# Performance work log

Measured on AMD Instinct MI355X. Metric: run time of the kernel, lower is better.

Reference implementation:

```python
import jax, jax.numpy as jnp
import numpy as np

B, N, DIN, D, NH, NL = 4, 256, 4, 64, 4, 2
DH = D // NH
EPS = 1e-5
SLOPE = 0.01  # torch LeakyReLU default negative_slope


def setup_inputs() -> dict:
    key = jax.random.key(0)
    ks = jax.random.split(key, 16)
    def p(k, shape, s=0.05):
        return jax.random.normal(k, shape, jnp.float32) * s
    return {
        "feature": jax.random.normal(ks[0], (B, N, N, DIN), jnp.float32),
        "W1": p(ks[1], (DIN, D)), "b1": jnp.zeros((D,), jnp.float32),
        "mw": p(ks[2], (NH, D)), "mb": jnp.zeros((NH,), jnp.float32),
        "bn_gamma": jnp.ones((D,), jnp.float32), "bn_beta": jnp.zeros((D,), jnp.float32),
        "Wq": p(ks[3], (NL, D, D)), "bq": jnp.zeros((NL, D), jnp.float32),
        "Wk": p(ks[4], (NL, D, D)), "bk": jnp.zeros((NL, D), jnp.float32),
        "Wv": p(ks[5], (NL, D, D)), "bv": jnp.zeros((NL, D), jnp.float32),
        "Wo": p(ks[6], (NL, D, D)), "bo": jnp.zeros((NL, D), jnp.float32),
        "ln1_g": jnp.ones((NL, D), jnp.float32), "ln1_b": jnp.zeros((NL, D), jnp.float32),
        "Wff1": p(ks[7], (NL, D, 2 * D)), "bff1": jnp.zeros((NL, 2 * D), jnp.float32),
        "Wff2": p(ks[8], (NL, 2 * D, D)), "bff2": jnp.zeros((NL, D), jnp.float32),
        "ln2_g": jnp.ones((NL, D), jnp.float32), "ln2_b": jnp.zeros((NL, D), jnp.float32),
    }


def _leaky(x):
    return jnp.where(x >= 0, x, SLOPE * x)


def _layer_norm(x, g, b):
    m = x.mean(axis=-1, keepdims=True)
    v = x.var(axis=-1, keepdims=True)
    return g * (x - m) / jnp.sqrt(v + EPS) + b


def reference(feature, W1, b1, mw, mb, bn_gamma, bn_beta,
              Wq, bq, Wk, bk, Wv, bv, Wo, bo, ln1_g, ln1_b,
              Wff1, bff1, Wff2, bff2, ln2_g, ln2_b):
    # linear1: (B,N,N,DIN) -> (B,N,N,D)
    feat = feature @ W1 + b1
    # per-head scalar attention score over node pairs: (NH,B,N,N)
    s = jnp.einsum('bijh,nh->nbij', feat, mw) + mb[:, None, None, None]
    w = jnp.exp(_leaky(s))
    w = w / w.sum(axis=3, keepdims=True)  # softmax-like over second node dim j
    # weighted aggregation: sum over i, then mean over heads -> (B,N,D)
    h = jnp.einsum('nbij,bijh->bjh', w, feat) / NH
    # BatchNorm1d over channels D, stats over (B,N) (training-mode, biased var)
    m = h.mean(axis=(0, 1))
    v = h.var(axis=(0, 1))
    x = bn_gamma * (h - m) / jnp.sqrt(v + EPS) + bn_beta  # (B,N,D)
    # standard post-LN TransformerEncoder, NL layers
    scale = 1.0 / np.sqrt(DH).astype(np.float32)
    for l in range(NL):
        q = (x @ Wq[l] + bq[l]).reshape(B, N, NH, DH)
        k = (x @ Wk[l] + bk[l]).reshape(B, N, NH, DH)
        vv = (x @ Wv[l] + bv[l]).reshape(B, N, NH, DH)
        a = jax.nn.softmax(jnp.einsum('bqhd,bkhd->bhqk', q, k) * scale, axis=-1)
        o = jnp.einsum('bhqk,bkhd->bqhd', a, vv).reshape(B, N, D) @ Wo[l] + bo[l]
        x = _layer_norm(x + o, ln1_g[l], ln1_b[l])
        f = jax.nn.relu(x @ Wff1[l] + bff1[l]) @ Wff2[l] + bff2[l]
        x = _layer_norm(x + f, ln2_g[l], ln2_b[l])
    return x
```

## Files before the change

### kernel.cpp

```cpp
#include <hip/hip_runtime.h>
#include <math.h>

#define B 4
#define N 256
#define DIN 4
#define D 64
#define NH 4
#define NL 2
#define DH 16

constexpr float EPS = 1e-5f;
constexpr float SLOPE = 0.01f;

template <int NF4>
__device__ __forceinline__ void stage(float* dst, const float* src, int t) {
    int lane = t & 63, w = t >> 6;
#pragma unroll
    for (int i0 = 0; i0 < NF4; i0 += 512) {
        int base = i0 + w * 64;
        __builtin_amdgcn_global_load_lds(
            (const __attribute__((address_space(1))) void*)(src + 4 * (base + lane)),
            (__attribute__((address_space(3))) void*)(dst + 4 * base),
            16, 0, 0);
    }
}

__global__ void __launch_bounds__(256) k_rowsum(
    const float* __restrict__ feature, const float* __restrict__ W1,
    const float* __restrict__ b1, const float* __restrict__ mw,
    const float* __restrict__ mb, float* __restrict__ rs,
    float* __restrict__ bnacc ) {
    __shared__ float M[16];
    __shared__ float C[4];
    int t = threadIdx.x;
    int lane = t & 63, w = t >> 6;
    int cb = blockIdx.x;
    if (cb == 0 && t < 128) bnacc[t] = 0.f;
    if (t < 16) {
        int n = t >> 2, kk = t & 3;
        float s = 0.f;
        for (int d = 0; d < D; ++d) s += W1[kk * D + d] * mw[n * D + d];
        M[t] = s;
    } else if (t < 20) {
        int n = t - 16;
        float s = mb[n];
        for (int d = 0; d < D; ++d) s += b1[d] * mw[n * D + d];
        C[n] = s;
    }
    __syncthreads();

    int bi = cb * 4 + w;
    const float4* fb = (const float4*)(feature) + (size_t)bi * N;
    float sn[4] = {0.f, 0.f, 0.f, 0.f};
#pragma unroll
    for (int m = 0; m < 4; ++m) {
        float4 f = fb[lane + 64 * m];
#pragma unroll
        for (int n = 0; n < 4; ++n) {
            float s = C[n] + f.x * M[n*4+0] + f.y * M[n*4+1] + f.z * M[n*4+2] + f.w * M[n*4+3];
            s = (s >= 0.f) ? s : SLOPE * s;
            sn[n] += __expf(s);
        }
    }
#pragma unroll
    for (int n = 0; n < 4; ++n)
#pragma unroll
        for (int off = 32; off > 0; off >>= 1) sn[n] += __shfl_xor(sn[n], off);
    if (lane == 0) {
        float4 o = {sn[0], sn[1], sn[2], sn[3]};
        *(float4*)(rs + (size_t)bi * 4) = o;
    }
}

__global__ void __launch_bounds__(256) k_aggregate(
    const float* __restrict__ feature, const float* __restrict__ W1,
    const float* __restrict__ b1, const float* __restrict__ mw,
    const float* __restrict__ mb, const float* __restrict__ rs,
    float* __restrict__ h, float* __restrict__ bnacc) {
    __shared__ float M[16];
    __shared__ float C[4];
    __shared__ float part[80];
    __shared__ float gacc[20];
    __shared__ float hs[4][D];
    int t = threadIdx.x;
    int lane = t & 63, w = t >> 6;
    int cb = blockIdx.x;
    if (t < 16) {
        int n = t >> 2, kk = t & 3;
        float s = 0.f;
        for (int d = 0; d < D; ++d) s += W1[kk * D + d] * mw[n * D + d];
        M[t] = s;
    } else if (t < 20) {
        int n = t - 16;
        float s = mb[n];
        for (int d = 0; d < D; ++d) s += b1[d] * mw[n * D + d];
        C[n] = s;
    }
    __syncthreads();

    int b = cb >> 6, j0 = (cb & 63) * 4;
    int i = t;
    const float4* fb = (const float4*)(feature) + ((size_t)(b * N + i) * N + j0);
    float4 f[4];
#pragma unroll
    for (int jj = 0; jj < 4; ++jj) f[jj] = fb[jj];
    float4 r4 = *(const float4*)(rs + (size_t)(b * N + i) * 4);
    float rinv[4] = {1.f / r4.x, 1.f / r4.y, 1.f / r4.z, 1.f / r4.w};
    float acc[4][5];
#pragma unroll
    for (int jj = 0; jj < 4; ++jj) {
        float wbar = 0.f;
#pragma unroll
        for (int n = 0; n < 4; ++n) {
            float s = C[n] + f[jj].x * M[n*4+0] + f[jj].y * M[n*4+1] + f[jj].z * M[n*4+2] + f[jj].w * M[n*4+3];
            s = (s >= 0.f) ? s : SLOPE * s;
            wbar += __expf(s) * rinv[n];
        }
        wbar *= 0.25f;
        acc[jj][0] = wbar * f[jj].x; acc[jj][1] = wbar * f[jj].y;
        acc[jj][2] = wbar * f[jj].z; acc[jj][3] = wbar * f[jj].w;
        acc[jj][4] = wbar;
    }
#pragma unroll
    for (int jj = 0; jj < 4; ++jj)
#pragma unroll
        for (int c = 0; c < 5; ++c)
#pragma unroll
            for (int off = 32; off > 0; off >>= 1) acc[jj][c] += __shfl_xor(acc[jj][c], off);
    if (lane == 0) {
#pragma unroll
        for (int jj = 0; jj < 4; ++jj)
#pragma unroll
            for (int c = 0; c < 5; ++c) part[w * 20 + jj * 5 + c] = acc[jj][c];
    }
    __syncthreads();
    if (t < 20) gacc[t] = part[t] + part[20 + t] + part[40 + t] + part[60 + t];
    __syncthreads();
    float hv = gacc[w * 5 + 4] * b1[lane];
#pragma unroll
    for (int kk = 0; kk < 4; ++kk) hv += gacc[w * 5 + kk] * W1[kk * D + lane];
    h[((size_t)(b * N + j0 + w)) * D + lane] = hv;
    hs[w][lane] = hv;
    __syncthreads();
    if (w == 0) {
        float s = hs[0][lane] + hs[1][lane] + hs[2][lane] + hs[3][lane];
        float sq = hs[0][lane]*hs[0][lane] + hs[1][lane]*hs[1][lane]
                 + hs[2][lane]*hs[2][lane] + hs[3][lane]*hs[3][lane];
        atomicAdd(bnacc + lane, s);
        atomicAdd(bnacc + D + lane, sq);
    }
}

__global__ void __launch_bounds__(512, 2) k_qkv0(
    const float* __restrict__ h, const float* __restrict__ bnacc,
    const float* __restrict__ bn_g, const float* __restrict__ bn_b,
    const float* __restrict__ Wq, const float* __restrict__ bq,
    const float* __restrict__ Wk, const float* __restrict__ bk,
    const float* __restrict__ Wv, const float* __restrict__ bv,
    float* __restrict__ x, float* __restrict__ q,
    float* __restrict__ k, float* __restrict__ v) {
    __shared__ __align__(16) float xsh[4 * D];
    __shared__ __align__(16) float pp[8 * 192];
    __shared__ __align__(16) float WqL[D * D];
    __shared__ __align__(16) float WkL[D * D];
    __shared__ __align__(16) float WvL[D * D];
    int t = threadIdx.x;
    int lane = t & 63, w = t >> 6;
    int tok4 = w & 3, kh = w >> 2;
    int token = blockIdx.x * 4 + tok4;
    int b = token >> 8, n = token & (N - 1);
    int ch = lane;

    stage<D * D / 4>(WqL, Wq, t);
    stage<D * D / 4>(WkL, Wk, t);
    stage<D * D / 4>(WvL, Wv, t);

    float mean = bnacc[ch] * (1.0f / (B * N));
    float var = bnacc[D + ch] * (1.0f / (B * N)) - mean * mean;
    float inv = rsqrtf(var + EPS);
    size_t xi = (size_t)token * D + ch;
    float xv = bn_g[ch] * (h[xi] - mean) * inv + bn_b[ch];
    float bq_r = bq[ch], bk_r = bk[ch], bv_r = bv[ch];
    if (kh == 0) {
        x[xi] = xv;
        xsh[tok4 * D + ch] = xv;
    }
    __syncthreads();

    const float4* xr4 = (const float4*)(xsh + tok4 * D + kh * 32);
    float aq0=0.f, aq1=0.f, ak0=0.f, ak1=0.f, av0=0.f, av1=0.f;
#pragma unroll
    for (int k4 = 0; k4 < 8; ++k4) {
        float4 xx = xr4[k4];
        int kk = kh * 32 + k4 * 4;
        aq0 += xx.x * WqL[(kk+0)*D+ch] + xx.z * WqL[(kk+2)*D+ch];
        aq1 += xx.y * WqL[(kk+1)*D+ch] + xx.w * WqL[(kk+3)*D+ch];
        ak0 += xx.x * WkL[(kk+0)*D+ch] + xx.z * WkL[(kk+2)*D+ch];
        ak1 += xx.y * WkL[(kk+1)*D+ch] + xx.w * WkL[(kk+3)*D+ch];
        av0 += xx.x * WvL[(kk+0)*D+ch] + xx.z * WvL[(kk+2)*D+ch];
        av1 += xx.y * WvL[(kk+1)*D+ch] + xx.w * WvL[(kk+3)*D+ch];
    }
    float* ppw = pp + w * 192;
    ppw[ch] = aq0 + aq1;
    ppw[64 + ch] = ak0 + ak1;
    ppw[128 + ch] = av0 + av1;
    __syncthreads();
    if (kh == 0) {
        int head = ch >> 4, dh = ch & (DH - 1);
        size_t oidx = (((size_t)(b * NH + head)) * N + n) * DH + dh;
        q[oidx] = bq_r + pp[tok4*192 + ch] + pp[(tok4+4)*192 + ch];
        k[oidx] = bk_r + pp[tok4*192 + 64 + ch] + pp[(tok4+4)*192 + 64 + ch];
        v[oidx] = bv_r + pp[tok4*192 + 128 + ch] + pp[(tok4+4)*192 + 128 + ch];
    }
}

__global__ void __launch_bounds__(512, 2) k_layer(
    const float* __restrict__ q, const float* __restrict__ k,
    const float* __restrict__ v,
    const float* __restrict__ Wo, const float* __restrict__ bo,
    const float* __restrict__ ln1g, const float* __restrict__ ln1b,
    const float* __restrict__ Wff1, const float* __restrict__ bff1,
    const float* __restrict__ Wff2, const float* __restrict__ bff2,
    const float* __restrict__ ln2g, const float* __restrict__ ln2b,
    const float* __restrict__ Wqn, const float* __restrict__ bqn,
    const float* __restrict__ Wkn, const float* __restrict__ bkn,
    const float* __restrict__ Wvn, const float* __restrict__ bvn,
    float* __restrict__ qo, float* __restrict__ ko, float* __restrict__ vo,
    float* __restrict__ x) {
    __shared__ __align__(16) float attS[4 * D];
    __shared__ __align__(16) float xs1[4 * D];
    __shared__ __align__(16) float f1s[4 * 2 * D];
    __shared__ __align__(16) float pp[8 * 192];
    __shared__ __align__(16) float WoL[D * D];
    __shared__ __align__(16) float Wff1L[D * 2 * D];
    __shared__ __align__(16) float Wff2L[2 * D * D];
    __shared__ __align__(16) float WqnL[D * D];
    __shared__ __align__(16) float WknL[D * D];
    __shared__ __align__(16) float WvnL[D * D];

    int t = threadIdx.x;
    int lane = t & 63, w = t >> 6;
    int b = blockIdx.x;
    int q0 = blockIdx.y * 4;
    int h_ = w & 3, qpair = w >> 2;
    int tok4 = w & 3, kh = w >> 2;
    int token = q0 + tok4;
    int ch = lane;

    int bh = b * NH + h_;
    const float* kb = k + (size_t)bh * N * DH;
    const float* vb = v + (size_t)bh * N * DH;
    float4 Kr[4][4], Vr[4][4];
#pragma unroll
    for (int j = 0; j < 4; ++j) {
        int key = lane + 64 * j;
#pragma unroll
        for (int c = 0; c < 4; ++c) {
            Kr[j][c] = *(const float4*)(kb + (size_t)key * DH + 4 * c);
            Vr[j][c] = *(const float4*)(vb + (size_t)key * DH + 4 * c);
        }
    }

    size_t xidx = ((size_t)b * N + token) * D + ch;
    float xv = x[xidx];
    float bo_r = bo[ch], l1g = ln1g[ch], l1b = ln1b[ch];
    float bf1_r = bff1[kh * D + ch];
    float bf2_r = bff2[ch], l2g = ln2g[ch], l2b = ln2b[ch];
    float bq_r = 0.f, bk_r = 0.f, bv_r = 0.f;
    if (Wqn != nullptr) { bq_r = bqn[ch]; bk_r = bkn[ch]; bv_r = bvn[ch]; }

    stage<1024>(WoL, Wo, t);
    stage<2048>(Wff1L, Wff1, t);
    stage<2048>(Wff2L, Wff2, t);
    if (Wqn != nullptr) {
        stage<1024>(WqnL, Wqn, t);
        stage<1024>(WknL, Wkn, t);
        stage<1024>(WvnL, Wvn, t);
    }

#pragma unroll
    for (int qq2 = 0; qq2 < 2; ++qq2) {
        int qq = qpair * 2 + qq2;
        const float* qp = q + ((size_t)bh * N + q0 + qq) * DH;
        float sq[DH];
#pragma unroll
        for (int d = 0; d < DH; ++d) sq[d] = qp[d];
        float s[4];
#pragma unroll
        for (int j = 0; j < 4; ++j) {
            float a = 0.f;
#pragma unroll
            for (int c = 0; c < 4; ++c)
                a += sq[4*c+0]*Kr[j][c].x + sq[4*c+1]*Kr[j][c].y +
                     sq[4*c+2]*Kr[j][c].z + sq[4*c+3]*Kr[j][c].w;
            s[j] = a;
        }
        float m = fmaxf(fmaxf(s[0], s[1]), fmaxf(s[2], s[3]));
#pragma unroll
        for (int off = 32; off > 0; off >>= 1) m = fmaxf(m, __shfl_xor(m, off));
        float p[4], lsum = 0.f;
#pragma unroll
        for (int j = 0; j < 4; ++j) { p[j] = __expf((s[j] - m) * 0.25f); lsum += p[j]; }
#pragma unroll
        for (int off = 32; off > 0; off >>= 1) lsum += __shfl_xor(lsum, off);
        float o[DH];
#pragma unroll
        for (int d = 0; d < DH; ++d) o[d] = 0.f;
#pragma unroll
        for (int j = 0; j < 4; ++j) {
#pragma unroll
            for (int c = 0; c < 4; ++c) {
                o[4*c+0] += p[j] * Vr[j][c].x;
                o[4*c+1] += p[j] * Vr[j][c].y;
                o[4*c+2] += p[j] * Vr[j][c].z;
                o[4*c+3] += p[j] * Vr[j][c].w;
            }
        }
#pragma unroll
        for (int d = 0; d < DH; ++d) {
#pragma unroll
            for (int off = 32; off > 0; off >>= 1) o[d] += __shfl_xor(o[d], off);
        }
        if (lane == 0) {
            float rl = 1.f / lsum;
#pragma unroll
            for (int d = 0; d < DH; ++d) attS[qq * D + h_ * DH + d] = o[d] * rl;
        }
    }
    __syncthreads();

    float* ppw = pp + w * 192;
    {
        const float4* ar4 = (const float4*)(attS + tok4 * D + kh * 32);
        float a0=0.f, a1=0.f, a2=0.f, a3=0.f;
#pragma unroll
        for (int k4 = 0; k4 < 8; ++k4) {
            float4 av = ar4[k4];
            int kk = kh * 32 + k4 * 4;
            a0 += av.x * WoL[(kk+0)*D+ch];
            a1 += av.y * WoL[(kk+1)*D+ch];
            a2 += av.z * WoL[(kk+2)*D+ch];
            a3 += av.w * WoL[(kk+3)*D+ch];
        }
        ppw[ch] = (a0+a1)+(a2+a3);
    }
    __syncthreads();
    float oo = bo_r + pp[tok4*192 + ch] + pp[(tok4+4)*192 + ch];
    float r = xv + oo;
    float s1 = r, sq1 = r * r;
#pragma unroll
    for (int off = 32; off > 0; off >>= 1) {
        s1 += __shfl_xor(s1, off);
        sq1 += __shfl_xor(sq1, off);
    }
    float mean1 = s1 * (1.0f / D);
    float var1 = sq1 * (1.0f / D) - mean1 * mean1;
    float x1 = l1g * (r - mean1) * rsqrtf(var1 + EPS) + l1b;
    if (kh == 0) xs1[tok4 * D + ch] = x1;
    __syncthreads();

    {
        const float4* xr4 = (const float4*)(xs1 + tok4 * D + kh * 32);
        float u0=0.f,u1=0.f,u2=0.f,u3=0.f, g0=0.f,g1=0.f,g2=0.f,g3=0.f;
#pragma unroll
        for (int k4 = 0; k4 < 8; ++k4) {
            float4 xx = xr4[k4];
            int kk = kh * 32 + k4 * 4;
            u0 += xx.x * Wff1L[(kk+0)*128+ch];
            u1 += xx.y * Wff1L[(kk+1)*128+ch];
            u2 += xx.z * Wff1L[(kk+2)*128+ch];
            u3 += xx.w * Wff1L[(kk+3)*128+ch];
            g0 += xx.x * Wff1L[(kk+0)*128+64+ch];
            g1 += xx.y * Wff1L[(kk+1)*128+64+ch];
            g2 += xx.z * Wff1L[(kk+2)*128+64+ch];
            g3 += xx.w * Wff1L[(kk+3)*128+64+ch];
        }
        ppw[ch] = (u0+u1)+(u2+u3);
        ppw[64+ch] = (g0+g1)+(g2+g3);
    }
    __syncthreads();
    f1s[tok4*128 + kh*64 + ch] =
        fmaxf(pp[tok4*192 + kh*64 + ch] + pp[(tok4+4)*192 + kh*64 + ch] + bf1_r, 0.f);
    __syncthreads();

    {
        const float4* fr4 = (const float4*)(f1s + tok4*128 + kh*64);
        float e0=0.f,e1=0.f,e2=0.f,e3=0.f;
#pragma unroll
        for (int k4 = 0; k4 < 16; ++k4) {
            float4 fv = fr4[k4];
            int kk = kh*64 + k4*4;
            e0 += fv.x * Wff2L[(kk+0)*D+ch];
            e1 += fv.y * Wff2L[(kk+1)*D+ch];
            e2 += fv.z * Wff2L[(kk+2)*D+ch];
            e3 += fv.w * Wff2L[(kk+3)*D+ch];
        }
        ppw[ch] = (e0+e1)+(e2+e3);
    }
    __syncthreads();
    float o2 = bf2_r + pp[tok4*192 + ch] + pp[(tok4+4)*192 + ch];
    float r2 = x1 + o2;
    float s2 = r2, sq2 = r2 * r2;
#pragma unroll
    for (int off = 32; off > 0; off >>= 1) {
        s2 += __shfl_xor(s2, off);
        sq2 += __shfl_xor(sq2, off);
    }
    float mean2 = s2 * (1.0f / D);
    float var2 = sq2 * (1.0f / D) - mean2 * mean2;
    float xnew = l2g * (r2 - mean2) * rsqrtf(var2 + EPS) + l2b;
    if (kh == 0) x[xidx] = xnew;

    if (Wqn != nullptr) {
        if (kh == 0) attS[tok4 * D + ch] = xnew;
        __syncthreads();
        const float4* xr4 = (const float4*)(attS + tok4 * D + kh * 32);
        float aq0=0.f, aq1=0.f, ak0=0.f, ak1=0.f, av0=0.f, av1=0.f;
#pragma unroll
        for (int k4 = 0; k4 < 8; ++k4) {
            float4 xx = xr4[k4];
            int kk = kh * 32 + k4 * 4;
            aq0 += xx.x * WqnL[(kk+0)*D+ch] + xx.z * WqnL[(kk+2)*D+ch];
            aq1 += xx.y * WqnL[(kk+1)*D+ch] + xx.w * WqnL[(kk+3)*D+ch];
            ak0 += xx.x * WknL[(kk+0)*D+ch] + xx.z * WknL[(kk+2)*D+ch];
            ak1 += xx.y * WknL[(kk+1)*D+ch] + xx.w * WknL[(kk+3)*D+ch];
            av0 += xx.x * WvnL[(kk+0)*D+ch] + xx.z * WvnL[(kk+2)*D+ch];
            av1 += xx.y * WvnL[(kk+1)*D+ch] + xx.w * WvnL[(kk+3)*D+ch];
        }
        ppw[ch] = aq0 + aq1;
        ppw[64+ch] = ak0 + ak1;
        ppw[128+ch] = av0 + av1;
        __syncthreads();
        if (kh == 0) {
            int head = ch >> 4, dh = ch & (DH - 1);
            size_t oidx = (((size_t)(b * NH + head)) * N + token) * DH + dh;
            qo[oidx] = bq_r + pp[tok4*192 + ch] + pp[(tok4+4)*192 + ch];
            ko[oidx] = bk_r + pp[tok4*192 + 64 + ch] + pp[(tok4+4)*192 + 64 + ch];
            vo[oidx] = bv_r + pp[tok4*192 + 128 + ch] + pp[(tok4+4)*192 + 128 + ch];
        }
    }
}

extern "C" void kernel_launch(void* const* d_in, const int* in_sizes, int n_in,
                              void* d_out, int out_size, void* d_ws, size_t ws_size,
                              hipStream_t stream) {
    const float* feature = (const float*)d_in[0];
    const float* W1   = (const float*)d_in[1];
    const float* b1   = (const float*)d_in[2];
    const float* mw   = (const float*)d_in[3];
    const float* mb   = (const float*)d_in[4];
    const float* bn_g = (const float*)d_in[5];
    const float* bn_b = (const float*)d_in[6];
    const float* Wq   = (const float*)d_in[7];
    const float* bq   = (const float*)d_in[8];
    const float* Wk   = (const float*)d_in[9];
    const float* bk   = (const float*)d_in[10];
    const float* Wv   = (const float*)d_in[11];
    const float* bv   = (const float*)d_in[12];
    const float* Wo   = (const float*)d_in[13];
    const float* bo   = (const float*)d_in[14];
    const float* ln1g = (const float*)d_in[15];
    const float* ln1b = (const float*)d_in[16];
    const float* Wff1 = (const float*)d_in[17];
    const float* bff1 = (const float*)d_in[18];
    const float* Wff2 = (const float*)d_in[19];
    const float* bff2 = (const float*)d_in[20];
    const float* ln2g = (const float*)d_in[21];
    const float* ln2b = (const float*)d_in[22];

    float* ws    = (float*)d_ws;
    float* rs    = ws;
    float* h     = rs + B * N * NH;
    float* bnacc = h + B * N * D;
    float* q     = bnacc + 128;
    float* k     = q + B * N * D;
    float* v     = k + B * N * D;
    float* x     = (float*)d_out;

    k_rowsum<<<256, 256, 0, stream>>>(feature, W1, b1, mw, mb, rs, bnacc);
    k_aggregate<<<256, 256, 0, stream>>>(feature, W1, b1, mw, mb, rs, h, bnacc);
    k_qkv0<<<256, 512, 0, stream>>>(h, bnacc, bn_g, bn_b,
                                    Wq, bq, Wk, bk, Wv, bv, x, q, k, v);
    k_layer<<<dim3(B, N / 4), 512, 0, stream>>>(q, k, v,
        Wo, bo, ln1g, ln1b, Wff1, bff1, Wff2, bff2, ln2g, ln2b,
        Wq + (size_t)D * D, bq + D, Wk + (size_t)D * D, bk + D,
        Wv + (size_t)D * D, bv + D, q, k, v, x);
    k_layer<<<dim3(B, N / 4), 512, 0, stream>>>(q, k, v,
        Wo + (size_t)D * D, bo + D, ln1g + D, ln1b + D,
        Wff1 + (size_t)D * 2 * D, bff1 + 2 * D,
        Wff2 + (size_t)2 * D * D, bff2 + D, ln2g + D, ln2b + D,
        nullptr, nullptr, nullptr, nullptr, nullptr, nullptr,
        nullptr, nullptr, nullptr, x);
}
```

Measured before the change: 147.8 us.

## Double threads in rowsum/aggregate and split attention keys across waves

Result: slower. 156.5 us (+5.9%).

```diff
diff --git a/kernel.cpp b/kernel.cpp
--- a/kernel.cpp
+++ b/kernel.cpp
@@ -25,13 +25,14 @@
     }
 }
 
-__global__ void __launch_bounds__(256) k_rowsum(
+__global__ void __launch_bounds__(512) k_rowsum(
     const float* __restrict__ feature, const float* __restrict__ W1,
     const float* __restrict__ b1, const float* __restrict__ mw,
     const float* __restrict__ mb, float* __restrict__ rs,
     float* __restrict__ bnacc ) {
     __shared__ float M[16];
     __shared__ float C[4];
+    __shared__ float part[32];
     int t = threadIdx.x;
     int lane = t & 63, w = t >> 6;
     int cb = blockIdx.x;
@@ -49,12 +50,13 @@
     }
     __syncthreads();
 
-    int bi = cb * 4 + w;
+    int r = w & 3, mh = w >> 2;
+    int bi = cb * 4 + r;
     const float4* fb = (const float4*)(feature) + (size_t)bi * N;
     float sn[4] = {0.f, 0.f, 0.f, 0.f};
 #pragma unroll
-    for (int m = 0; m < 4; ++m) {
-        float4 f = fb[lane + 64 * m];
+    for (int mm = 0; mm < 2; ++mm) {
+        float4 f = fb[lane + 64 * (mh * 2 + mm)];
 #pragma unroll
         for (int n = 0; n < 4; ++n) {
             float s = C[n] + f.x * M[n*4+0] + f.y * M[n*4+1] + f.z * M[n*4+2] + f.w * M[n*4+3];
@@ -67,19 +69,24 @@
 #pragma unroll
         for (int off = 32; off > 0; off >>= 1) sn[n] += __shfl_xor(sn[n], off);
     if (lane == 0) {
-        float4 o = {sn[0], sn[1], sn[2], sn[3]};
-        *(float4*)(rs + (size_t)bi * 4) = o;
+#pragma unroll
+        for (int n = 0; n < 4; ++n) part[w * 4 + n] = sn[n];
+    }
+    __syncthreads();
+    if (t < 16) {
+        int rr = t >> 2, n = t & 3;
+        rs[((size_t)(cb * 4 + rr)) * 4 + n] = part[rr * 4 + n] + part[(rr + 4) * 4 + n];
     }
 }
 
-__global__ void __launch_bounds__(256) k_aggregate(
+__global__ void __launch_bounds__(512) k_aggregate(
     const float* __restrict__ feature, const float* __restrict__ W1,
     const float* __restrict__ b1, const float* __restrict__ mw,
     const float* __restrict__ mb, const float* __restrict__ rs,
     float* __restrict__ h, float* __restrict__ bnacc) {
     __shared__ float M[16];
     __shared__ float C[4];
-    __shared__ float part[80];
+    __shared__ float part[8][10];
     __shared__ float gacc[20];
     __shared__ float hs[4][D];
     int t = threadIdx.x;
@@ -99,16 +106,16 @@
     __syncthreads();
 
     int b = cb >> 6, j0 = (cb & 63) * 4;
-    int i = t;
-    const float4* fb = (const float4*)(feature) + ((size_t)(b * N + i) * N + j0);
-    float4 f[4];
-#pragma unroll
-    for (int jj = 0; jj < 4; ++jj) f[jj] = fb[jj];
+    int i = t & 255, jh = t >> 8;
+    const float4* fb = (const float4*)(feature) + ((size_t)(b * N + i) * N + j0 + jh * 2);
+    float4 f[2];
+    f[0] = fb[0];
+    f[1] = fb[1];
     float4 r4 = *(const float4*)(rs + (size_t)(b * N + i) * 4);
     float rinv[4] = {1.f / r4.x, 1.f / r4.y, 1.f / r4.z, 1.f / r4.w};
-    float acc[4][5];
-#pragma unroll
-    for (int jj = 0; jj < 4; ++jj) {
+    float acc[2][5];
+#pragma unroll
+    for (int jj = 0; jj < 2; ++jj) {
         float wbar = 0.f;
 #pragma unroll
         for (int n = 0; n < 4; ++n) {
@@ -122,27 +129,34 @@
         acc[jj][4] = wbar;
     }
 #pragma unroll
-    for (int jj = 0; jj < 4; ++jj)
+    for (int jj = 0; jj < 2; ++jj)
 #pragma unroll
         for (int c = 0; c < 5; ++c)
 #pragma unroll
             for (int off = 32; off > 0; off >>= 1) acc[jj][c] += __shfl_xor(acc[jj][c], off);
     if (lane == 0) {
 #pragma unroll
-        for (int jj = 0; jj < 4; ++jj)
-#pragma unroll
-            for (int c = 0; c < 5; ++c) part[w * 20 + jj * 5 + c] = acc[jj][c];
-    }
-    __syncthreads();
-    if (t < 20) gacc[t] = part[t] + part[20 + t] + part[40 + t] + part[60 + t];
-    __syncthreads();
-    float hv = gacc[w * 5 + 4] * b1[lane];
-#pragma unroll
-    for (int kk = 0; kk < 4; ++kk) hv += gacc[w * 5 + kk] * W1[kk * D + lane];
-    h[((size_t)(b * N + j0 + w)) * D + lane] = hv;
-    hs[w][lane] = hv;
-    __syncthreads();
-    if (w == 0) {
+        for (int jj = 0; jj < 2; ++jj)
+#pragma unroll
+            for (int c = 0; c < 5; ++c) part[w][jj * 5 + c] = acc[jj][c];
+    }
+    __syncthreads();
+    if (t < 20) {
+        int jj = t / 5, c = t - jj * 5;
+        int g = jj >> 1, jjl = jj & 1;
+        gacc[t] = part[g*4+0][jjl*5+c] + part[g*4+1][jjl*5+c]
+                + part[g*4+2][jjl*5+c] + part[g*4+3][jjl*5+c];
+    }
+    __syncthreads();
+    if (t < 256) {
+        float hv = gacc[w * 5 + 4] * b1[lane];
+#pragma unroll
+        for (int kk = 0; kk < 4; ++kk) hv += gacc[w * 5 + kk] * W1[kk * D + lane];
+        h[((size_t)(b * N + j0 + w)) * D + lane] = hv;
+        hs[w][lane] = hv;
+    }
+    __syncthreads();
+    if (t < 64) {
         float s = hs[0][lane] + hs[1][lane] + hs[2][lane] + hs[3][lane];
         float sq = hs[0][lane]*hs[0][lane] + hs[1][lane]*hs[1][lane]
                  + hs[2][lane]*hs[2][lane] + hs[3][lane]*hs[3][lane];
@@ -231,6 +245,9 @@
     __shared__ __align__(16) float xs1[4 * D];
     __shared__ __align__(16) float f1s[4 * 2 * D];
     __shared__ __align__(16) float pp[8 * 192];
+    __shared__ __align__(16) float attO[2][4 * D];
+    __shared__ float attM[2][16];
+    __shared__ float attL[2][16];
     __shared__ __align__(16) float WoL[D * D];
     __shared__ __align__(16) float Wff1L[D * 2 * D];
     __shared__ __align__(16) float Wff2L[2 * D * D];
@@ -242,23 +259,30 @@
     int lane = t & 63, w = t >> 6;
     int b = blockIdx.x;
     int q0 = blockIdx.y * 4;
-    int h_ = w & 3, qpair = w >> 2;
+    int h_ = w & 3, half = w >> 2;
     int tok4 = w & 3, kh = w >> 2;
     int token = q0 + tok4;
     int ch = lane;
 
     int bh = b * NH + h_;
-    const float* kb = k + (size_t)bh * N * DH;
-    const float* vb = v + (size_t)bh * N * DH;
-    float4 Kr[4][4], Vr[4][4];
-#pragma unroll
-    for (int j = 0; j < 4; ++j) {
+    const float* kb = k + ((size_t)bh * N + half * 128) * DH;
+    const float* vb = v + ((size_t)bh * N + half * 128) * DH;
+    float4 Kr[2][4], Vr[2][4];
+#pragma unroll
+    for (int j = 0; j < 2; ++j) {
         int key = lane + 64 * j;
 #pragma unroll
         for (int c = 0; c < 4; ++c) {
             Kr[j][c] = *(const float4*)(kb + (size_t)key * DH + 4 * c);
             Vr[j][c] = *(const float4*)(vb + (size_t)key * DH + 4 * c);
         }
+    }
+    float4 qv[4][4];
+#pragma unroll
+    for (int qq = 0; qq < 4; ++qq) {
+        const float4* qp4 = (const float4*)(q + ((size_t)bh * N + q0 + qq) * DH);
+#pragma unroll
+        for (int c = 0; c < 4; ++c) qv[qq][c] = qp4[c];
     }
 
     size_t xidx = ((size_t)b * N + token) * D + ch;
@@ -279,42 +303,30 @@
     }
 
 #pragma unroll
-    for (int qq2 = 0; qq2 < 2; ++qq2) {
-        int qq = qpair * 2 + qq2;
-        const float* qp = q + ((size_t)bh * N + q0 + qq) * DH;
-        float sq[DH];
-#pragma unroll
-        for (int d = 0; d < DH; ++d) sq[d] = qp[d];
-        float s[4];
-#pragma unroll
-        for (int j = 0; j < 4; ++j) {
-            float a = 0.f;
-#pragma unroll
-            for (int c = 0; c < 4; ++c)
-                a += sq[4*c+0]*Kr[j][c].x + sq[4*c+1]*Kr[j][c].y +
-                     sq[4*c+2]*Kr[j][c].z + sq[4*c+3]*Kr[j][c].w;
-            s[j] = a;
-        }
-        float m = fmaxf(fmaxf(s[0], s[1]), fmaxf(s[2], s[3]));
+    for (int qq = 0; qq < 4; ++qq) {
+        float s0 = 0.f, s1 = 0.f;
+#pragma unroll
+        for (int c = 0; c < 4; ++c) {
+            s0 += qv[qq][c].x * Kr[0][c].x + qv[qq][c].y * Kr[0][c].y +
+                  qv[qq][c].z * Kr[0][c].z + qv[qq][c].w * Kr[0][c].w;
+            s1 += qv[qq][c].x * Kr[1][c].x + qv[qq][c].y * Kr[1][c].y +
+                  qv[qq][c].z * Kr[1][c].z + qv[qq][c].w * Kr[1][c].w;
+        }
+        float m = fmaxf(s0, s1);
 #pragma unroll
         for (int off = 32; off > 0; off >>= 1) m = fmaxf(m, __shfl_xor(m, off));
-        float p[4], lsum = 0.f;
-#pragma unroll
-        for (int j = 0; j < 4; ++j) { p[j] = __expf((s[j] - m) * 0.25f); lsum += p[j]; }
+        float p0 = __expf((s0 - m) * 0.25f);
+        float p1 = __expf((s1 - m) * 0.25f);
+        float lsum = p0 + p1;
 #pragma unroll
         for (int off = 32; off > 0; off >>= 1) lsum += __shfl_xor(lsum, off);
         float o[DH];
 #pragma unroll
-        for (int d = 0; d < DH; ++d) o[d] = 0.f;
-#pragma unroll
-        for (int j = 0; j < 4; ++j) {
-#pragma unroll
-            for (int c = 0; c < 4; ++c) {
-                o[4*c+0] += p[j] * Vr[j][c].x;
-                o[4*c+1] += p[j] * Vr[j][c].y;
-                o[4*c+2] += p[j] * Vr[j][c].z;
-                o[4*c+3] += p[j] * Vr[j][c].w;
-            }
+        for (int c = 0; c < 4; ++c) {
+            o[4*c+0] = p0 * Vr[0][c].x + p1 * Vr[1][c].x;
+            o[4*c+1] = p0 * Vr[0][c].y + p1 * Vr[1][c].y;
+            o[4*c+2] = p0 * Vr[0][c].z + p1 * Vr[1][c].z;
+            o[4*c+3] = p0 * Vr[0][c].w + p1 * Vr[1][c].w;
         }
 #pragma unroll
         for (int d = 0; d < DH; ++d) {
@@ -322,10 +334,24 @@
             for (int off = 32; off > 0; off >>= 1) o[d] += __shfl_xor(o[d], off);
         }
         if (lane == 0) {
-            float rl = 1.f / lsum;
-#pragma unroll
-            for (int d = 0; d < DH; ++d) attS[qq * D + h_ * DH + d] = o[d] * rl;
-        }
+#pragma unroll
+            for (int d = 0; d < DH; ++d) attO[half][qq * D + h_ * DH + d] = o[d];
+            attM[half][qq * 4 + h_] = m;
+            attL[half][qq * 4 + h_] = lsum;
+        }
+    }
+    __syncthreads();
+
+    if (w < 4) {
+        int qq = w;
+        int head = ch >> 4;
+        float m0 = attM[0][qq * 4 + head], m1 = attM[1][qq * 4 + head];
+        float l0 = attL[0][qq * 4 + head], l1 = attL[1][qq * 4 + head];
+        float M = fmaxf(m0, m1);
+        float e0 = __expf((m0 - M) * 0.25f);
+        float e1 = __expf((m1 - M) * 0.25f);
+        float rl = 1.f / (l0 * e0 + l1 * e1);
+        attS[qq * D + ch] = (attO[0][qq * D + ch] * e0 + attO[1][qq * D + ch] * e1) * rl;
     }
     __syncthreads();
 
@@ -477,8 +503,8 @@
     float* v     = k + B * N * D;
     float* x     = (float*)d_out;
 
-    k_rowsum<<<256, 256, 0, stream>>>(feature, W1, b1, mw, mb, rs, bnacc);
-    k_aggregate<<<256, 256, 0, stream>>>(feature, W1, b1, mw, mb, rs, h, bnacc);
+    k_rowsum<<<256, 512, 0, stream>>>(feature, W1, b1, mw, mb, rs, bnacc);
+    k_aggregate<<<256, 512, 0, stream>>>(feature, W1, b1, mw, mb, rs, h, bnacc);
     k_qkv0<<<256, 512, 0, stream>>>(h, bnacc, bn_g, bn_b,
                                     Wq, bq, Wk, bk, Wv, bv, x, q, k, v);
     k_layer<<<dim3(B, N / 4), 512, 0, stream>>>(q, k, v,
```
